# Kernel optimization log

Hardware: AMD Instinct MI355X
Metric: run time of the kernel (lower is better)

## Reference

```python
import jax, jax.numpy as jnp
import numpy as np

NBITS = 8
MAXQ = float(2**NBITS - 1)  # 255 for uint8 asymmetric quantization


def asym_quantize(x):
    """Per-tensor asymmetric quantization to the [0, 255] grid.

    x ~ scale * (q - zero), with scale = (max-min)/255, zero = round(-min/scale).
    Returns (q, scale, zero) with q kept in float32 holding integer values.
    """
    xmax = jnp.max(x)
    xmin = jnp.min(x)
    scale = (xmax - xmin) / MAXQ
    zero = jnp.round(-xmin / scale)
    q = jnp.clip(jnp.round(x / scale) + zero, 0.0, MAXQ)
    return q, scale, zero


def setup_inputs() -> dict:
    key = jax.random.key(0)
    kA, kB = jax.random.split(key)
    A = jax.random.normal(kA, (4096, 2048), dtype=jnp.float32)
    B = jax.random.normal(kB, (2048, 4096), dtype=jnp.float32)
    return {"A": A, "B": B}


def reference(A, B):
    # Quantize both operands per-tensor asymmetrically.
    qA, sA, zA = asym_quantize(A)  # [M, K]
    qB, sB, zB = asym_quantize(B)  # [K, N]
    K = A.shape[1]

    # Integer GEMM on the quantized values (exact int accumulation in int32).
    acc = jnp.matmul(qA.astype(jnp.int32), qB.astype(jnp.int32)).astype(jnp.float32)  # [M, N]

    # Fused asymmetric dequant epilogue:
    # A @ B = sA*sB * (qA@qB - zA * colsum(qB) - zB * rowsum(qA) + K*zA*zB)
    rowsum_qA = jnp.sum(qA, axis=1, keepdims=True)   # [M, 1]
    colsum_qB = jnp.sum(qB, axis=0, keepdims=True)   # [1, N]
    out = (sA * sB) * (acc - zA * colsum_qB - zB * rowsum_qA
                       + jnp.float32(K) * zA * zB)
    return out
```

## Files before the change

### kernel.cpp

```cpp
#include <hip/hip_runtime.h>
#include <math.h>


#define M_DIM 4096
#define K_DIM 2048
#define N_DIM 4096

using int4v = __attribute__((ext_vector_type(4))) int;

typedef __attribute__((address_space(1))) const void glb_cv;
typedef __attribute__((address_space(3))) void lds_v;

__device__ __forceinline__ int qbyte(float x, float s, float z) {
    float q = fminf(fmaxf(rintf(x / s) + z, 0.0f), 255.0f);
    return (int)q - 128;
}

__device__ __forceinline__ int sum4(int w) {
    return (int)(signed char)(w) + (int)(signed char)(w >> 8) +
           (int)(signed char)(w >> 16) + (int)(signed char)(w >> 24);
}

__global__ void minmax_stage1(const float* __restrict__ A,
                              const float* __restrict__ B,
                              float* __restrict__ partials) {
    int b = blockIdx.x;
    const float* src = (b < 512) ? A : B;
    int lb = (b < 512) ? b : b - 512;
    const float4* v = (const float4*)src + (long)lb * 4096;
    float mn = INFINITY, mx = -INFINITY;
    for (int i = threadIdx.x; i < 4096; i += 256) {
        float4 x = v[i];
        mn = fminf(mn, fminf(fminf(x.x, x.y), fminf(x.z, x.w)));
        mx = fmaxf(mx, fmaxf(fmaxf(x.x, x.y), fmaxf(x.z, x.w)));
    }
    for (int off = 32; off; off >>= 1) {
        mn = fminf(mn, __shfl_down(mn, off));
        mx = fmaxf(mx, __shfl_down(mx, off));
    }
    __shared__ float smn[4], smx[4];
    int w = threadIdx.x >> 6;
    if ((threadIdx.x & 63) == 0) { smn[w] = mn; smx[w] = mx; }
    __syncthreads();
    if (threadIdx.x == 0) {
        mn = fminf(fminf(smn[0], smn[1]), fminf(smn[2], smn[3]));
        mx = fmaxf(fmaxf(smx[0], smx[1]), fmaxf(smx[2], smx[3]));
        partials[2 * b] = mn;
        partials[2 * b + 1] = mx;
    }
}

__global__ void minmax_stage2(const float* __restrict__ partials,
                              float* __restrict__ qp,
                              int* __restrict__ colB) {
    int t = threadIdx.x;
    for (int i = t; i < N_DIM; i += 256) colB[i] = 0;
    float mnA = INFINITY, mxA = -INFINITY, mnB = INFINITY, mxB = -INFINITY;
    for (int i = t; i < 512; i += 256) {
        mnA = fminf(mnA, partials[2 * i]);
        mxA = fmaxf(mxA, partials[2 * i + 1]);
        mnB = fminf(mnB, partials[2 * (i + 512)]);
        mxB = fmaxf(mxB, partials[2 * (i + 512) + 1]);
    }
    for (int off = 32; off; off >>= 1) {
        mnA = fminf(mnA, __shfl_down(mnA, off));
        mxA = fmaxf(mxA, __shfl_down(mxA, off));
        mnB = fminf(mnB, __shfl_down(mnB, off));
        mxB = fmaxf(mxB, __shfl_down(mxB, off));
    }
    __shared__ float s[4][4];
    int w = t >> 6;
    if ((t & 63) == 0) { s[w][0] = mnA; s[w][1] = mxA; s[w][2] = mnB; s[w][3] = mxB; }
    __syncthreads();
    if (t == 0) {
        for (int i = 1; i < 4; i++) {
            mnA = fminf(mnA, s[i][0]); mxA = fmaxf(mxA, s[i][1]);
            mnB = fminf(mnB, s[i][2]); mxB = fmaxf(mxB, s[i][3]);
        }
        float sA = (mxA - mnA) / 255.0f;
        float zA = rintf(-mnA / sA);
        float sB = (mxB - mnB) / 255.0f;
        float zB = rintf(-mnB / sB);
        qp[0] = sA; qp[1] = zA; qp[2] = sB; qp[3] = zB;
    }
}

__global__ void quantA_kernel(const float* __restrict__ X,
                              signed char* __restrict__ Q,
                              const float* __restrict__ qp,
                              int* __restrict__ rowA) {
    float s = qp[0], z = qp[1];
    int t = threadIdx.x;
    long base = (long)blockIdx.x * 4096 + (long)t * 16;
    const float4* v = (const float4*)(X + base);
    union { signed char c[16]; int4 i4; } u;
    int ls = 0;
#pragma unroll
    for (int j = 0; j < 4; j++) {
        float4 x = v[j];
        int q0 = qbyte(x.x, s, z), q1 = qbyte(x.y, s, z);
        int q2 = qbyte(x.z, s, z), q3 = qbyte(x.w, s, z);
        u.c[j * 4 + 0] = (signed char)q0;
        u.c[j * 4 + 1] = (signed char)q1;
        u.c[j * 4 + 2] = (signed char)q2;
        u.c[j * 4 + 3] = (signed char)q3;
        ls += q0 + q1 + q2 + q3;
    }
    *(int4*)(Q + base) = u.i4;
    for (int off = 32; off; off >>= 1) ls += __shfl_down(ls, off);
    __shared__ int ws[4];
    if ((t & 63) == 0) ws[t >> 6] = ls;
    __syncthreads();
    if (t == 0) rowA[blockIdx.x * 2] = ws[0] + ws[1];
    if (t == 128) rowA[blockIdx.x * 2 + 1] = ws[2] + ws[3];
}

__global__ void quantBT_kernel(const float* __restrict__ B,
                               signed char* __restrict__ BT,
                               const float* __restrict__ qp,
                               int* __restrict__ colB) {
    __shared__ __align__(16) signed char tile[64][80];
    float s = qp[2], z = qp[3];
    int k0 = blockIdx.x * 64, n0 = blockIdx.y * 64;
    int t = threadIdx.x;
    int cn = (t & 15) * 4;
    int rk = t >> 4;
#pragma unroll
    for (int rr = 0; rr < 64; rr += 16) {
        int k = rk + rr;
        float4 x = *(const float4*)&B[(long)(k0 + k) * N_DIM + n0 + cn];
        tile[cn + 0][k] = (signed char)qbyte(x.x, s, z);
        tile[cn + 1][k] = (signed char)qbyte(x.y, s, z);
        tile[cn + 2][k] = (signed char)qbyte(x.z, s, z);
        tile[cn + 3][k] = (signed char)qbyte(x.w, s, z);
    }
    __syncthreads();
    int n2 = t >> 2, kc = (t & 3) * 16;
    int4 w = *(const int4*)&tile[n2][kc];
    *(int4*)&BT[(long)(n0 + n2) * K_DIM + k0 + kc] = w;
    int ls = sum4(w.x) + sum4(w.y) + sum4(w.z) + sum4(w.w);
    ls += __shfl_down(ls, 2);
    ls += __shfl_down(ls, 1);
    if ((t & 3) == 0) atomicAdd(&colB[n0 + n2], ls);
}

__global__ __launch_bounds__(256, 2) void gemm_i8(
        const signed char* __restrict__ A8,
        const signed char* __restrict__ B8T,
        const int* __restrict__ rowA,
        const int* __restrict__ colB,
        const float* __restrict__ qp,
        float* __restrict__ out) {
    __shared__ __align__(16) signed char As[256 * 64];
    __shared__ __align__(16) signed char Bs[128 * 64];

    int r0 = blockIdx.y * 256;
    int c0 = blockIdx.x * 128;
    int t = threadIdx.x, lane = t & 63, wave = t >> 6;

    int4v acc[8][4];
#pragma unroll
    for (int i = 0; i < 8; i++)
#pragma unroll
        for (int j = 0; j < 4; j++) acc[i][j] = (int4v){0, 0, 0, 0};

    int wm = (wave >> 1) * 128;
    int wn = (wave & 1) * 64;
    int mrow = lane & 15;
    int g = lane >> 4;
    int kq = ((g ^ ((mrow >> 1) & 3)) * 16);

    long aoff[4], boff[2];
#pragma unroll
    for (int j = 0; j < 4; j++) {
        int ch = t + 256 * j;
        int row = ch >> 2, c = ch & 3;
        int gk = c ^ ((row >> 1) & 3);
        aoff[j] = (long)(r0 + row) * K_DIM + gk * 16;
    }
#pragma unroll
    for (int j = 0; j < 2; j++) {
        int ch = t + 256 * j;
        int row = ch >> 2, c = ch & 3;
        int gk = c ^ ((row >> 1) & 3);
        boff[j] = (long)(c0 + row) * K_DIM + gk * 16;
    }

    for (int k0 = 0; k0 < K_DIM; k0 += 64) {
        __syncthreads();
#pragma unroll
        for (int j = 0; j < 4; j++)
            __builtin_amdgcn_global_load_lds((glb_cv*)(A8 + aoff[j] + k0),
                                             (lds_v*)(As + (t + 256 * j) * 16), 16, 0, 0);
#pragma unroll
        for (int j = 0; j < 2; j++)
            __builtin_amdgcn_global_load_lds((glb_cv*)(B8T + boff[j] + k0),
                                             (lds_v*)(Bs + (t + 256 * j) * 16), 16, 0, 0);
        __syncthreads();

        int4v af[8], bf[4];
#pragma unroll
        for (int i = 0; i < 8; i++)
            af[i] = *(const int4v*)&As[(wm + i * 16 + mrow) * 64 + kq];
#pragma unroll
        for (int j = 0; j < 4; j++)
            bf[j] = *(const int4v*)&Bs[(wn + j * 16 + mrow) * 64 + kq];
#pragma unroll
        for (int i = 0; i < 8; i++)
#pragma unroll
            for (int j = 0; j < 4; j++)
                acc[i][j] = __builtin_amdgcn_mfma_i32_16x16x64_i8(af[i], bf[j], acc[i][j], 0, 0, 0);
    }

    float sA = qp[0], zA = qp[1], sB = qp[2], zB = qp[3];
    int cA = 128 - (int)zA, cB = 128 - (int)zB;
    float ss = sA * sB;
    int Kzz = K_DIM * cA * cB;
    int ocol = c0 + wn + mrow;
    int orow = r0 + wm + g * 4;
#pragma unroll
    for (int i = 0; i < 8; i++) {
        int ra[4];
#pragma unroll
        for (int r = 0; r < 4; r++) ra[r] = cB * rowA[orow + i * 16 + r] + Kzz;
#pragma unroll
        for (int j = 0; j < 4; j++) {
            int cc = ocol + j * 16;
            int can = cA * colB[cc];
#pragma unroll
            for (int r = 0; r < 4; r++) {
                int v = acc[i][j][r] + ra[r] + can;
                out[(long)(orow + i * 16 + r) * N_DIM + cc] = ss * (float)v;
            }
        }
    }
}

extern "C" void kernel_launch(void* const* d_in, const int* in_sizes, int n_in,
                              void* d_out, int out_size, void* d_ws, size_t ws_size,
                              hipStream_t stream) {
    const float* A = (const float*)d_in[0];
    const float* B = (const float*)d_in[1];
    float* out = (float*)d_out;
    char* ws = (char*)d_ws;

    signed char* A8  = (signed char*)ws;
    signed char* B8T = (signed char*)(ws + 8388608);
    int*   rowA      = (int*)(ws + 16777216);
    int*   colB      = (int*)(ws + 16793600);
    float* partials  = (float*)(ws + 16809984);
    float* qp        = (float*)(ws + 16818176);

    minmax_stage1<<<1024, 256, 0, stream>>>(A, B, partials);
    minmax_stage2<<<1, 256, 0, stream>>>(partials, qp, colB);
    quantA_kernel<<<2048, 256, 0, stream>>>(A, A8, qp, rowA);
    quantBT_kernel<<<dim3(32, 64), 256, 0, stream>>>(B, B8T, qp, colB);
    gemm_i8<<<dim3(32, 16), 256, 0, stream>>>(A8, B8T, rowA, colB, qp, out);
}
```

Baseline: 170.0 us.

## Retile int8 GEMM to 128x128x128 with XCD-aware block mapping and reciprocal quantization

Changes the GEMM tile from 256x128 with K-step 64 to 128x128 with K-step 128 and a new XOR swizzle, raising the launch-bounds occupancy hint to 3. It launches a 1D grid with blocks remapped across the 8 XCDs for L2 locality. Quantization now multiplies by a precomputed reciprocal scale instead of dividing, and the B transpose packs four k-bytes per int in a padded int LDS tile. The reciprocal may round a few values differently from the reference division, and the smaller tile lowers arithmetic intensity per block.

```diff
diff --git a/kernel.cpp b/kernel.cpp
--- a/kernel.cpp
+++ b/kernel.cpp
@@ -11,8 +11,8 @@
 typedef __attribute__((address_space(1))) const void glb_cv;
 typedef __attribute__((address_space(3))) void lds_v;
 
-__device__ __forceinline__ int qbyte(float x, float s, float z) {
-    float q = fminf(fmaxf(rintf(x / s) + z, 0.0f), 255.0f);
+__device__ __forceinline__ int qbyte(float x, float rs, float z) {
+    float q = fminf(fmaxf(rintf(x * rs) + z, 0.0f), 255.0f);
     return (int)q - 128;
 }
 
@@ -82,6 +82,7 @@
         float sB = (mxB - mnB) / 255.0f;
         float zB = rintf(-mnB / sB);
         qp[0] = sA; qp[1] = zA; qp[2] = sB; qp[3] = zB;
+        qp[4] = 1.0f / sA; qp[5] = 1.0f / sB;
     }
 }
 
@@ -89,7 +90,7 @@
                               signed char* __restrict__ Q,
                               const float* __restrict__ qp,
                               int* __restrict__ rowA) {
-    float s = qp[0], z = qp[1];
+    float rs = qp[4], z = qp[1];
     int t = threadIdx.x;
     long base = (long)blockIdx.x * 4096 + (long)t * 16;
     const float4* v = (const float4*)(X + base);
@@ -98,8 +99,8 @@
 #pragma unroll
     for (int j = 0; j < 4; j++) {
         float4 x = v[j];
-        int q0 = qbyte(x.x, s, z), q1 = qbyte(x.y, s, z);
-        int q2 = qbyte(x.z, s, z), q3 = qbyte(x.w, s, z);
+        int q0 = qbyte(x.x, rs, z), q1 = qbyte(x.y, rs, z);
+        int q2 = qbyte(x.z, rs, z), q3 = qbyte(x.w, rs, z);
         u.c[j * 4 + 0] = (signed char)q0;
         u.c[j * 4 + 1] = (signed char)q1;
         u.c[j * 4 + 2] = (signed char)q2;
@@ -119,97 +120,111 @@
                                signed char* __restrict__ BT,
                                const float* __restrict__ qp,
                                int* __restrict__ colB) {
-    __shared__ __align__(16) signed char tile[64][80];
-    float s = qp[2], z = qp[3];
+    __shared__ int tile[64][17];
+    float rs = qp[5], z = qp[3];
     int k0 = blockIdx.x * 64, n0 = blockIdx.y * 64;
     int t = threadIdx.x;
     int cn = (t & 15) * 4;
-    int rk = t >> 4;
-#pragma unroll
-    for (int rr = 0; rr < 64; rr += 16) {
-        int k = rk + rr;
-        float4 x = *(const float4*)&B[(long)(k0 + k) * N_DIM + n0 + cn];
-        tile[cn + 0][k] = (signed char)qbyte(x.x, s, z);
-        tile[cn + 1][k] = (signed char)qbyte(x.y, s, z);
-        tile[cn + 2][k] = (signed char)qbyte(x.z, s, z);
-        tile[cn + 3][k] = (signed char)qbyte(x.w, s, z);
-    }
-    __syncthreads();
-    int n2 = t >> 2, kc = (t & 3) * 16;
-    int4 w = *(const int4*)&tile[n2][kc];
-    *(int4*)&BT[(long)(n0 + n2) * K_DIM + k0 + kc] = w;
-    int ls = sum4(w.x) + sum4(w.y) + sum4(w.z) + sum4(w.w);
+    int kg = (t >> 4) * 4;
+    int w0 = 0, w1 = 0, w2 = 0, w3 = 0;
+#pragma unroll
+    for (int r = 0; r < 4; r++) {
+        float4 x = *(const float4*)&B[(long)(k0 + kg + r) * N_DIM + n0 + cn];
+        w0 |= (qbyte(x.x, rs, z) & 255) << (8 * r);
+        w1 |= (qbyte(x.y, rs, z) & 255) << (8 * r);
+        w2 |= (qbyte(x.z, rs, z) & 255) << (8 * r);
+        w3 |= (qbyte(x.w, rs, z) & 255) << (8 * r);
+    }
+    int kc = kg >> 2;
+    tile[cn + 0][kc] = w0;
+    tile[cn + 1][kc] = w1;
+    tile[cn + 2][kc] = w2;
+    tile[cn + 3][kc] = w3;
+    __syncthreads();
+    int n2 = t >> 2, kb = (t & 3) * 4;
+    int4 v;
+    v.x = tile[n2][kb + 0];
+    v.y = tile[n2][kb + 1];
+    v.z = tile[n2][kb + 2];
+    v.w = tile[n2][kb + 3];
+    *(int4*)&BT[(long)(n0 + n2) * K_DIM + k0 + (t & 3) * 16] = v;
+    int ls = sum4(v.x) + sum4(v.y) + sum4(v.z) + sum4(v.w);
     ls += __shfl_down(ls, 2);
     ls += __shfl_down(ls, 1);
     if ((t & 3) == 0) atomicAdd(&colB[n0 + n2], ls);
 }
 
-__global__ __launch_bounds__(256, 2) void gemm_i8(
+__global__ __launch_bounds__(256, 3) void gemm_i8(
         const signed char* __restrict__ A8,
         const signed char* __restrict__ B8T,
         const int* __restrict__ rowA,
         const int* __restrict__ colB,
         const float* __restrict__ qp,
         float* __restrict__ out) {
-    __shared__ __align__(16) signed char As[256 * 64];
-    __shared__ __align__(16) signed char Bs[128 * 64];
-
-    int r0 = blockIdx.y * 256;
-    int c0 = blockIdx.x * 128;
+    __shared__ __align__(16) signed char As[128 * 128];
+    __shared__ __align__(16) signed char Bs[128 * 128];
+
+    int b = blockIdx.x;
+    int xcd = b & 7, i0 = b >> 3;
+    int r = xcd + 8 * (i0 >> 6);
+    int j = i0 & 63;
+    int mt = (r >> 2) * 8 + (j >> 3);
+    int nt = (r & 3) * 8 + (j & 7);
+    int r0 = mt * 128, c0 = nt * 128;
+
     int t = threadIdx.x, lane = t & 63, wave = t >> 6;
-
-    int4v acc[8][4];
-#pragma unroll
-    for (int i = 0; i < 8; i++)
-#pragma unroll
-        for (int j = 0; j < 4; j++) acc[i][j] = (int4v){0, 0, 0, 0};
-
-    int wm = (wave >> 1) * 128;
-    int wn = (wave & 1) * 64;
     int mrow = lane & 15;
     int g = lane >> 4;
-    int kq = ((g ^ ((mrow >> 1) & 3)) * 16);
-
-    long aoff[4], boff[2];
-#pragma unroll
-    for (int j = 0; j < 4; j++) {
-        int ch = t + 256 * j;
-        int row = ch >> 2, c = ch & 3;
-        int gk = c ^ ((row >> 1) & 3);
-        aoff[j] = (long)(r0 + row) * K_DIM + gk * 16;
-    }
-#pragma unroll
-    for (int j = 0; j < 2; j++) {
-        int ch = t + 256 * j;
-        int row = ch >> 2, c = ch & 3;
-        int gk = c ^ ((row >> 1) & 3);
-        boff[j] = (long)(c0 + row) * K_DIM + gk * 16;
-    }
-
-    for (int k0 = 0; k0 < K_DIM; k0 += 64) {
+    int wm = (wave >> 1) * 64;
+    int wn = (wave & 1) * 64;
+
+    int4v acc[4][4];
+#pragma unroll
+    for (int i = 0; i < 4; i++)
+#pragma unroll
+        for (int jj = 0; jj < 4; jj++) acc[i][jj] = (int4v){0, 0, 0, 0};
+
+    long aoff[4], boff[4];
+#pragma unroll
+    for (int jj = 0; jj < 4; jj++) {
+        int ch = t + 256 * jj;
+        int row = ch >> 3, p = ch & 7;
+        int gk = p ^ (row & 7);
+        aoff[jj] = (long)(r0 + row) * K_DIM + gk * 16;
+        boff[jj] = (long)(c0 + row) * K_DIM + gk * 16;
+    }
+
+    int swz = (mrow & 7);
+
+    for (int k0 = 0; k0 < K_DIM; k0 += 128) {
         __syncthreads();
 #pragma unroll
-        for (int j = 0; j < 4; j++)
-            __builtin_amdgcn_global_load_lds((glb_cv*)(A8 + aoff[j] + k0),
-                                             (lds_v*)(As + (t + 256 * j) * 16), 16, 0, 0);
-#pragma unroll
-        for (int j = 0; j < 2; j++)
-            __builtin_amdgcn_global_load_lds((glb_cv*)(B8T + boff[j] + k0),
-                                             (lds_v*)(Bs + (t + 256 * j) * 16), 16, 0, 0);
+        for (int jj = 0; jj < 4; jj++)
+            __builtin_amdgcn_global_load_lds((glb_cv*)(A8 + aoff[jj] + k0),
+                                             (lds_v*)(As + (t + 256 * jj) * 16), 16, 0, 0);
+#pragma unroll
+        for (int jj = 0; jj < 4; jj++)
+            __builtin_amdgcn_global_load_lds((glb_cv*)(B8T + boff[jj] + k0),
+                                             (lds_v*)(Bs + (t + 256 * jj) * 16), 16, 0, 0);
         __syncthreads();
 
-        int4v af[8], bf[4];
-#pragma unroll
-        for (int i = 0; i < 8; i++)
-            af[i] = *(const int4v*)&As[(wm + i * 16 + mrow) * 64 + kq];
-#pragma unroll
-        for (int j = 0; j < 4; j++)
-            bf[j] = *(const int4v*)&Bs[(wn + j * 16 + mrow) * 64 + kq];
-#pragma unroll
-        for (int i = 0; i < 8; i++)
-#pragma unroll
-            for (int j = 0; j < 4; j++)
-                acc[i][j] = __builtin_amdgcn_mfma_i32_16x16x64_i8(af[i], bf[j], acc[i][j], 0, 0, 0);
+#pragma unroll
+        for (int ks = 0; ks < 2; ks++) {
+            int c = ks * 4 + g;
+            int koff = (c ^ swz) * 16;
+            int4v af[4], bf[4];
+#pragma unroll
+            for (int i = 0; i < 4; i++)
+                af[i] = *(const int4v*)&As[(wm + i * 16 + mrow) * 128 + koff];
+#pragma unroll
+            for (int jj = 0; jj < 4; jj++)
+                bf[jj] = *(const int4v*)&Bs[(wn + jj * 16 + mrow) * 128 + koff];
+#pragma unroll
+            for (int i = 0; i < 4; i++)
+#pragma unroll
+                for (int jj = 0; jj < 4; jj++)
+                    acc[i][jj] = __builtin_amdgcn_mfma_i32_16x16x64_i8(af[i], bf[jj], acc[i][jj], 0, 0, 0);
+        }
     }
 
     float sA = qp[0], zA = qp[1], sB = qp[2], zB = qp[3];
@@ -219,18 +234,18 @@
     int ocol = c0 + wn + mrow;
     int orow = r0 + wm + g * 4;
 #pragma unroll
-    for (int i = 0; i < 8; i++) {
+    for (int i = 0; i < 4; i++) {
         int ra[4];
 #pragma unroll
-        for (int r = 0; r < 4; r++) ra[r] = cB * rowA[orow + i * 16 + r] + Kzz;
-#pragma unroll
-        for (int j = 0; j < 4; j++) {
-            int cc = ocol + j * 16;
+        for (int rr = 0; rr < 4; rr++) ra[rr] = cB * rowA[orow + i * 16 + rr] + Kzz;
+#pragma unroll
+        for (int jj = 0; jj < 4; jj++) {
+            int cc = ocol + jj * 16;
             int can = cA * colB[cc];
 #pragma unroll
-            for (int r = 0; r < 4; r++) {
-                int v = acc[i][j][r] + ra[r] + can;
-                out[(long)(orow + i * 16 + r) * N_DIM + cc] = ss * (float)v;
+            for (int rr = 0; rr < 4; rr++) {
+                int v = acc[i][jj][rr] + ra[rr] + can;
+                out[(long)(orow + i * 16 + rr) * N_DIM + cc] = ss * (float)v;
             }
         }
     }
@@ -255,5 +270,5 @@
     minmax_stage2<<<1, 256, 0, stream>>>(partials, qp, colB);
     quantA_kernel<<<2048, 256, 0, stream>>>(A, A8, qp, rowA);
     quantBT_kernel<<<dim3(32, 64), 256, 0, stream>>>(B, B8T, qp, colB);
-    gemm_i8<<<dim3(32, 16), 256, 0, stream>>>(A8, B8T, rowA, colB, qp, out);
-}
+    gemm_i8<<<1024, 256, 0, stream>>>(A8, B8T, rowA, colB, qp, out);
+}
```

Result: faster. 162.9 us (-4.2%).
